# Performance work log

Measured on AMD Instinct MI355X. Metric: run time of the kernel, lower is better.

## Reference

```python
import jax, jax.numpy as jnp
import numpy as np
from jax import lax

EPS = 1e-5


def _conv3x3(inp, w):
    # NCHW input, OIHW kernel, VALID padding, stride 1 (matches nn.Conv2d(k=3, s=1, p=0))
    return lax.conv_general_dilated(inp, w, (1, 1), 'VALID',
                                    dimension_numbers=('NCHW', 'OIHW', 'NCHW'))


def _bn(h, gamma, beta, mean, var):
    # inference-mode BatchNorm2d
    inv = gamma / jnp.sqrt(var + EPS)
    return h * inv[None, :, None, None] + (beta - mean * inv)[None, :, None, None]


def _xcorr_depthwise(zf, xf):
    # per-sample, per-channel sliding cross-correlation: template zf over search xf
    B, C, Hz, Wz = zf.shape
    _, _, Hx, Wx = xf.shape
    xr = xf.reshape(1, B * C, Hx, Wx)
    kr = zf.reshape(B * C, 1, Hz, Wz)
    out = lax.conv_general_dilated(xr, kr, (1, 1), 'VALID',
                                   feature_group_count=B * C,
                                   dimension_numbers=('NCHW', 'OIHW', 'NCHW'))
    return out.reshape(B, C, out.shape[2], out.shape[3])


def setup_inputs() -> dict:
    key = jax.random.key(0)
    ks = jax.random.split(key, 12)
    B, Cin, Ch = 64, 256, 256
    z = jax.random.normal(ks[0], (B, Cin, 16, 16), dtype=jnp.float32)
    x = jax.random.normal(ks[1], (B, Cin, 32, 32), dtype=jnp.float32)
    # conv weights ~ N(0, 0.01) as in _initialize_weights
    w_z = 0.01 * jax.random.normal(ks[2], (Ch, Cin, 3, 3), dtype=jnp.float32)
    w_x = 0.01 * jax.random.normal(ks[3], (Ch, Cin, 3, 3), dtype=jnp.float32)
    gamma_z = 0.5 + jax.random.uniform(ks[4], (Ch,), dtype=jnp.float32)
    beta_z = 0.1 * jax.random.normal(ks[5], (Ch,), dtype=jnp.float32)
    mean_z = 0.1 * jax.random.normal(ks[6], (Ch,), dtype=jnp.float32)
    var_z = 0.5 + jax.random.uniform(ks[7], (Ch,), dtype=jnp.float32)
    gamma_x = 0.5 + jax.random.uniform(ks[8], (Ch,), dtype=jnp.float32)
    beta_x = 0.1 * jax.random.normal(ks[9], (Ch,), dtype=jnp.float32)
    mean_x = 0.1 * jax.random.normal(ks[10], (Ch,), dtype=jnp.float32)
    var_x = 0.5 + jax.random.uniform(ks[11], (Ch,), dtype=jnp.float32)
    return {'z': z, 'x': x, 'w_z': w_z, 'w_x': w_x,
            'gamma_z': gamma_z, 'beta_z': beta_z, 'mean_z': mean_z, 'var_z': var_z,
            'gamma_x': gamma_x, 'beta_x': beta_x, 'mean_x': mean_x, 'var_x': var_x}


def reference(z, x, w_z, w_x, gamma_z, beta_z, mean_z, var_z,
              gamma_x, beta_x, mean_x, var_x):
    zf = _bn(_conv3x3(z, w_z), gamma_z, beta_z, mean_z, var_z)   # [B,C,14,14]
    xf = _bn(_conv3x3(x, w_x), gamma_x, beta_x, mean_x, var_x)   # [B,C,30,30]
    return _xcorr_depthwise(zf, xf)                               # [B,C,17,17]
```

## Files before the change

### kernel.cpp

```cpp
#include <hip/hip_runtime.h>
#include <cstdint>
#include <cstddef>

typedef _Float16 f16;
typedef _Float16 half4 __attribute__((ext_vector_type(4)));
typedef _Float16 half8 __attribute__((ext_vector_type(8)));
typedef __fp16 fp16x2 __attribute__((ext_vector_type(2)));
typedef float f32x4 __attribute__((ext_vector_type(4)));

#define BN_EPS 1e-5f

#if defined(__has_builtin)
# if __has_builtin(__builtin_amdgcn_fdot2)
#  define HAVE_FDOT2 1
# endif
#endif
#ifndef HAVE_FDOT2
# define HAVE_FDOT2 0
#endif

static constexpr size_t OFF_XB  = 0;
static constexpr size_t OFF_ZB  = 33554432;
static constexpr size_t OFF_WX  = 41943040;
static constexpr size_t OFF_WZ  = 43122688;
static constexpr size_t OFF_BNX = 44302336;
static constexpr size_t OFF_BNZ = 44304384;
static constexpr size_t OFF_XFH = 44306432;
static constexpr size_t OFF_ZFH = 75763712;

__global__ __launch_bounds__(256) void prep_all(
    const float* __restrict__ x, const float* __restrict__ z,
    const float* __restrict__ w_x, const float* __restrict__ w_z,
    const float* __restrict__ gx, const float* __restrict__ bx,
    const float* __restrict__ mx, const float* __restrict__ vx,
    const float* __restrict__ gz, const float* __restrict__ bz,
    const float* __restrict__ mz, const float* __restrict__ vz,
    f16* __restrict__ xb, f16* __restrict__ zb,
    f16* __restrict__ wxA, f16* __restrict__ wzA,
    float* __restrict__ bnx, float* __restrict__ bnz) {
  __shared__ float tile[64][33];
  __shared__ alignas(16) f16 wtile[2304];
  const int bid = blockIdx.x;
  const int tid = threadIdx.x;
  if (bid < 12288) {
    const float* src; f16* dst; int lw, r;
    if (bid < 8192) { src = x; dst = xb; lw = 5; r = bid; }
    else            { src = z; dst = zb; lw = 4; r = bid - 8192; }
    const int W = 1 << lw;
    const int c0 = (r & 3) << 6;
    const int h = (r >> 2) & (W - 1);
    const int b = (r >> 2) >> lw;
    const float* sp = src + ((size_t)((b << 8) + c0) << (2 * lw)) + ((size_t)h << lw);
    const int w4 = W >> 2;
    const int n1 = w4 << 6;
    for (int i = tid; i < n1; i += 256) {
      int cl = i >> (lw - 2), c4 = i & (w4 - 1);
      float4 v = *(const float4*)(sp + ((size_t)cl << (2 * lw)) + (c4 << 2));
      int w0 = c4 << 2;
      tile[cl][w0] = v.x; tile[cl][w0 + 1] = v.y;
      tile[cl][w0 + 2] = v.z; tile[cl][w0 + 3] = v.w;
    }
    __syncthreads();
    f16* dp = dst + ((size_t)((b << lw) + h) << lw << 8) + c0;
    const int n2 = W << 3;
    for (int j = tid; j < n2; j += 256) {
      int w = j >> 3, cl0 = (j & 7) << 3;
      half8 o;
#pragma unroll
      for (int e = 0; e < 8; ++e) o[e] = (f16)tile[cl0 + e][w];
      *(half8*)(dp + (w << 8) + cl0) = o;
    }
  } else if (bid < 12800) {
    int r = bid - 12288;
    const float* src = (r < 256) ? w_x : w_z;
    f16* dst = (r < 256) ? wxA : wzA;
    int cout = r & 255;
    const float* sp = src + (size_t)cout * 2304;
    for (int i = tid; i < 2304; i += 256) {
      int cin = i / 9, khw = i - cin * 9;
      wtile[khw * 256 + cin] = (f16)sp[i];
    }
    __syncthreads();
    for (int c = tid; c < 288; c += 256) {
      int khw = c >> 5, cin0 = (c & 31) << 3;
      *(half8*)(dst + (khw << 16) + (cout << 8) + cin0) =
          *(const half8*)(wtile + khw * 256 + cin0);
    }
  } else {
    int c = tid;
    float iv = gx[c] / sqrtf(vx[c] + BN_EPS);
    bnx[c] = iv;
    bnx[256 + c] = bx[c] - mx[c] * iv;
    float iz = gz[c] / sqrtf(vz[c] + BN_EPS);
    bnz[c] = iz;
    bnz[256 + c] = bz[c] - mz[c] * iz;
  }
}

__device__ __forceinline__ void gl_lds16(const f16* g, f16* l) {
  __builtin_amdgcn_global_load_lds((__attribute__((address_space(1))) void*)g,
                                   (__attribute__((address_space(3))) void*)l, 16, 0, 0);
}

__global__ __launch_bounds__(256, 4) void conv_gemm_u(
    const f16* __restrict__ xb, const f16* __restrict__ zb,
    const f16* __restrict__ wx, const f16* __restrict__ wz,
    const float* __restrict__ bnx, const float* __restrict__ bnz,
    f16* __restrict__ xfh, f16* __restrict__ zfh) {
  __shared__ f16 As[128 * 64];
  __shared__ f16 Bs[128 * 64];
  const int g = blockIdx.x;
  const int pairIdx = ((g >> 4) << 3) | (g & 7);
  const int mblk = (g >> 3) & 1;
  if (pairIdx >= 548) return;
  const f16* inp; const f16* wA; const float* bn; f16* out;
  int nblk, HIN, WIN, WOUT, NPIX, WPAD, OPLANE;
  if (pairIdx < 450) {
    inp = xb; wA = wx; bn = bnx; out = xfh; nblk = pairIdx;
    HIN = 32; WIN = 32; WOUT = 30; NPIX = 900; WPAD = 32; OPLANE = 960;
  } else {
    inp = zb; wA = wz; bn = bnz; out = zfh; nblk = pairIdx - 450;
    HIN = 16; WIN = 16; WOUT = 14; NPIX = 196; WPAD = 16; OPLANE = 224;
  }
  const int tid = threadIdx.x;
  const int wid = tid >> 6, lane = tid & 63;
  const int wm = (wid >> 1) << 6, wn = (wid & 1) << 6;
  const int q = lane >> 4, lm = lane & 15;
  const int sr = lane >> 3, sc = lane & 7;
  const int swz = (sc ^ sr) << 3;
  const int mbase = mblk << 7;

  int arow[4], brow[4];
#pragma unroll
  for (int l = 0; l < 4; ++l) {
    int rr = (wid << 5) + (l << 3) + sr;
    arow[l] = ((mbase + rr) << 8) + swz;
    int n = (nblk << 7) + rr;
    int b = n / NPIX, rem = n - b * NPIX;
    int oh = rem / WOUT, ow = rem - oh * WOUT;
    brow[l] = (((b * HIN + oh) * WIN + ow) << 8) + swz;
  }

  f32x4 acc[4][4] = {};
  const int cA0 = (q ^ (lm & 7)) << 3;

  for (int kt = 0; kt < 36; ++kt) {
    const int cinb = kt / 9;
    const int khw = kt - cinb * 9;
    const int cin0 = cinb << 6;
    const int kh = khw / 3, kw = khw - kh * 3;
    const int wofs = (khw << 16) + cin0;
    const int iofs = ((kh * WIN + kw) << 8) + cin0;
#pragma unroll
    for (int l = 0; l < 4; ++l) {
      const int ldso = ((wid << 5) + (l << 3)) << 6;
      gl_lds16(wA + wofs + arow[l], As + ldso);
      gl_lds16(inp + iofs + brow[l], Bs + ldso);
    }
    __syncthreads();
#pragma unroll
    for (int h = 0; h < 2; ++h) {
      const int co = cA0 ^ (h << 5);
      half8 af[4], bf[4];
#pragma unroll
      for (int f = 0; f < 4; ++f) {
        af[f] = *(const half8*)&As[((wm + (f << 4) + lm) << 6) + co];
        bf[f] = *(const half8*)&Bs[((wn + (f << 4) + lm) << 6) + co];
      }
#pragma unroll
      for (int fm = 0; fm < 4; ++fm)
#pragma unroll
        for (int fn = 0; fn < 4; ++fn)
          acc[fm][fn] =
              __builtin_amdgcn_mfma_f32_16x16x32_f16(af[fm], bf[fn], acc[fm][fn], 0, 0, 0);
    }
    __syncthreads();
  }

#pragma unroll
  for (int fn = 0; fn < 4; ++fn) {
    int n_g = (nblk << 7) + wn + (fn << 4) + lm;
    int b = n_g / NPIX, rem = n_g - b * NPIX;
    int oh = rem / WOUT, ow = rem - oh * WOUT;
    f16* op = out + (size_t)(b << 8) * OPLANE + oh * WPAD + ow;
#pragma unroll
    for (int fm = 0; fm < 4; ++fm) {
      int m0 = mbase + wm + (fm << 4) + (q << 2);
#pragma unroll
      for (int rg = 0; rg < 4; ++rg) {
        int m = m0 + rg;
        op[(size_t)m * OPLANE] = (f16)(acc[fm][fn][rg] * bn[m] + bn[256 + m]);
      }
    }
  }
}

static constexpr int XROWS = 30;
static constexpr int XSTR  = 40;
static constexpr int XCHN  = XROWS * XSTR;
static constexpr int ZCHN  = 224;
static constexpr int CPB   = 15;

__global__ __launch_bounds__(256) void xcorr_dw3(const f16* __restrict__ zfh,
                                                 const f16* __restrict__ xfh,
                                                 float* __restrict__ out) {
  __shared__ alignas(16) f16 xs[CPB * XCHN];
  __shared__ alignas(16) f16 zs[CPB * ZCHN];
  const int t = threadIdx.x;
  const int ch0 = blockIdx.x * CPB;

  for (int i = t; i < CPB * 30 * 4; i += 256) {
    int ch = i / 120, rem = i - ch * 120;
    int row = rem >> 2, c8 = (rem & 3) << 3;
    if (ch0 + ch < 16384)
      *(half8*)(xs + ch * XCHN + row * XSTR + c8) =
          *(const half8*)(xfh + (size_t)(ch0 + ch) * 960 + row * 32 + c8);
  }
  for (int i = t; i < CPB * 28; i += 256) {
    int ch = i / 28, rem = i - ch * 28;
    if (ch0 + ch < 16384)
      *(half8*)(zs + ch * ZCHN + rem * 8) =
          *(const half8*)(zfh + (size_t)(ch0 + ch) * 224 + rem * 8);
  }
  __syncthreads();

  int lc = t / 17;
  const int oy = t - lc * 17;
  const bool ok = (lc < CPB) && (ch0 + lc < 16384);
  if (lc >= CPB) lc = CPB - 1;
  const f16* xbp = xs + lc * XCHN;
  const f16* zbp = zs + lc * ZCHN;

  float acc[17];
#pragma unroll
  for (int j = 0; j < 17; ++j) acc[j] = 0.f;

#if HAVE_FDOT2
  union X32 { half8 v8[4]; fp16x2 h2[16]; };
  union Z16 { half8 v8[2]; fp16x2 h2[8]; };
  for (int u = 0; u < 14; ++u) {
    X32 xl;
#pragma unroll
    for (int k = 0; k < 4; ++k)
      xl.v8[k] = *(const half8*)(xbp + (oy + u) * XSTR + (k << 3));
    Z16 zl;
    zl.v8[0] = *(const half8*)(zbp + u * 16);
    zl.v8[1] = *(const half8*)(zbp + u * 16 + 8);
    fp16x2 xo[15];
#pragma unroll
    for (int m = 0; m < 15; ++m) { xo[m][0] = xl.h2[m][1]; xo[m][1] = xl.h2[m + 1][0]; }
#pragma unroll
    for (int m = 0; m < 7; ++m) {
#pragma unroll
      for (int tt = 0; tt < 8; ++tt) {
        acc[2 * tt]     = __builtin_amdgcn_fdot2(zl.h2[m], xl.h2[m + tt], acc[2 * tt], false);
        acc[2 * tt + 1] = __builtin_amdgcn_fdot2(zl.h2[m], xo[m + tt],    acc[2 * tt + 1], false);
      }
      acc[16] = __builtin_amdgcn_fdot2(zl.h2[m], xl.h2[m + 8], acc[16], false);
    }
  }
#else
  for (int u = 0; u < 14; ++u) {
    float xr[30];
#pragma unroll
    for (int k = 0; k < 4; ++k) {
      half8 h = *(const half8*)(xbp + (oy + u) * XSTR + (k << 3));
#pragma unroll
      for (int e = 0; e < 8; ++e)
        if (k * 8 + e < 30) xr[k * 8 + e] = (float)h[e];
    }
    float zc[14];
    {
      half8 z0 = *(const half8*)(zbp + u * 16);
      half8 z1 = *(const half8*)(zbp + u * 16 + 8);
#pragma unroll
      for (int e = 0; e < 8; ++e) zc[e] = (float)z0[e];
#pragma unroll
      for (int e = 0; e < 6; ++e) zc[8 + e] = (float)z1[e];
    }
#pragma unroll
    for (int v = 0; v < 14; ++v)
#pragma unroll
      for (int j = 0; j < 17; ++j) acc[j] = fmaf(zc[v], xr[v + j], acc[j]);
  }
#endif

  if (ok) {
    float* op = out + (size_t)(ch0 + lc) * 289 + oy * 17;
#pragma unroll
    for (int j = 0; j < 17; ++j) op[j] = acc[j];
  }
}

extern "C" void kernel_launch(void* const* d_in, const int* in_sizes, int n_in,
                              void* d_out, int out_size, void* d_ws, size_t ws_size,
                              hipStream_t stream) {
  const float* z = (const float*)d_in[0];
  const float* x = (const float*)d_in[1];
  const float* w_z = (const float*)d_in[2];
  const float* w_x = (const float*)d_in[3];
  const float* gamma_z = (const float*)d_in[4];
  const float* beta_z = (const float*)d_in[5];
  const float* mean_z = (const float*)d_in[6];
  const float* var_z = (const float*)d_in[7];
  const float* gamma_x = (const float*)d_in[8];
  const float* beta_x = (const float*)d_in[9];
  const float* mean_x = (const float*)d_in[10];
  const float* var_x = (const float*)d_in[11];

  char* ws = (char*)d_ws;
  f16* xb = (f16*)(ws + OFF_XB);
  f16* zb = (f16*)(ws + OFF_ZB);
  f16* wxA = (f16*)(ws + OFF_WX);
  f16* wzA = (f16*)(ws + OFF_WZ);
  float* bnx = (float*)(ws + OFF_BNX);
  float* bnz = (float*)(ws + OFF_BNZ);
  f16* xfh = (f16*)(ws + OFF_XFH);
  f16* zfh = (f16*)(ws + OFF_ZFH);
  float* out = (float*)d_out;

  prep_all<<<12801, 256, 0, stream>>>(x, z, w_x, w_z,
                                      gamma_x, beta_x, mean_x, var_x,
                                      gamma_z, beta_z, mean_z, var_z,
                                      xb, zb, wxA, wzA, bnx, bnz);

  conv_gemm_u<<<1104, 256, 0, stream>>>(xb, zb, wxA, wzA, bnx, bnz, xfh, zfh);

  xcorr_dw3<<<(16384 + CPB - 1) / CPB, 256, 0, stream>>>(zfh, xfh, out);
}
```

Baseline: 276.0 us.

## Stage input row band once per cin block and reuse across 3x3 taps

The implicit-GEMM conv now loads a contiguous band of input pixel rows (256 rows x 64 channels) into LDS once per 64-channel block. All 9 kernel taps are served from that band by shifting row offsets, so the input is no longer reloaded per tap. Weights are read straight from global memory into registers instead of going through LDS. Tiles are now per batch and row segment, which gives 1280 blocks with tail masking, and launch bounds are lowered to 3 waves per SIMD. This trades more LDS per block and more global weight traffic for far fewer input loads and barriers.

```diff
diff --git a/kernel.cpp b/kernel.cpp
--- a/kernel.cpp
+++ b/kernel.cpp
@@ -102,94 +102,112 @@
                                    (__attribute__((address_space(3))) void*)l, 16, 0, 0);
 }
 
-__global__ __launch_bounds__(256, 4) void conv_gemm_u(
+__global__ __launch_bounds__(256, 3) void conv_gemm_u(
     const f16* __restrict__ xb, const f16* __restrict__ zb,
     const f16* __restrict__ wx, const f16* __restrict__ wz,
     const float* __restrict__ bnx, const float* __restrict__ bnz,
     f16* __restrict__ xfh, f16* __restrict__ zfh) {
-  __shared__ f16 As[128 * 64];
-  __shared__ f16 Bs[128 * 64];
+  __shared__ alignas(16) f16 Bs[256 * 64];
   const int g = blockIdx.x;
   const int pairIdx = ((g >> 4) << 3) | (g & 7);
   const int mblk = (g >> 3) & 1;
-  if (pairIdx >= 548) return;
   const f16* inp; const f16* wA; const float* bn; f16* out;
-  int nblk, HIN, WIN, WOUT, NPIX, WPAD, OPLANE;
-  if (pairIdx < 450) {
-    inp = xb; wA = wx; bn = bnx; out = xfh; nblk = pairIdx;
+  int b, t, HIN, WIN, WOUT, NPIX, WPAD, OPLANE;
+  if (pairIdx < 512) {
+    inp = xb; wA = wx; bn = bnx; out = xfh;
+    b = pairIdx >> 3; t = pairIdx & 7;
     HIN = 32; WIN = 32; WOUT = 30; NPIX = 900; WPAD = 32; OPLANE = 960;
   } else {
-    inp = zb; wA = wz; bn = bnz; out = zfh; nblk = pairIdx - 450;
+    int r = pairIdx - 512;
+    inp = zb; wA = wz; bn = bnz; out = zfh;
+    b = r >> 1; t = r & 1;
     HIN = 16; WIN = 16; WOUT = 14; NPIX = 196; WPAD = 16; OPLANE = 224;
   }
   const int tid = threadIdx.x;
   const int wid = tid >> 6, lane = tid & 63;
   const int wm = (wid >> 1) << 6, wn = (wid & 1) << 6;
   const int q = lane >> 4, lm = lane & 15;
-  const int sr = lane >> 3, sc = lane & 7;
-  const int swz = (sc ^ sr) << 3;
   const int mbase = mblk << 7;
 
-  int arow[4], brow[4];
-#pragma unroll
-  for (int l = 0; l < 4; ++l) {
-    int rr = (wid << 5) + (l << 3) + sr;
-    arow[l] = ((mbase + rr) << 8) + swz;
-    int n = (nblk << 7) + rr;
-    int b = n / NPIX, rem = n - b * NPIX;
-    int oh = rem / WOUT, ow = rem - oh * WOUT;
-    brow[l] = (((b * HIN + oh) * WIN + ow) << 8) + swz;
-  }
+  const int ih0 = (t << 7) / WOUT;
+  const int pix0 = b * HIN * WIN + ih0 * WIN;
+
+  int inrow[4];
+#pragma unroll
+  for (int fn = 0; fn < 4; ++fn) {
+    int n_out = (t << 7) + wn + (fn << 4) + lm;
+    int v = n_out < NPIX ? n_out : NPIX - 1;
+    int oh = v / WOUT, ow = v - oh * WOUT;
+    inrow[fn] = (oh - ih0) * WIN + ow;
+  }
+
+  const f16* Abase = wA + ((mbase + wm + lm) << 8) + (q << 3);
 
   f32x4 acc[4][4] = {};
-  const int cA0 = (q ^ (lm & 7)) << 3;
-
-  for (int kt = 0; kt < 36; ++kt) {
-    const int cinb = kt / 9;
-    const int khw = kt - cinb * 9;
-    const int cin0 = cinb << 6;
-    const int kh = khw / 3, kw = khw - kh * 3;
-    const int wofs = (khw << 16) + cin0;
-    const int iofs = ((kh * WIN + kw) << 8) + cin0;
-#pragma unroll
-    for (int l = 0; l < 4; ++l) {
-      const int ldso = ((wid << 5) + (l << 3)) << 6;
-      gl_lds16(wA + wofs + arow[l], As + ldso);
-      gl_lds16(inp + iofs + brow[l], Bs + ldso);
-    }
+  const int cb0 = q << 4;
+  const int cb1 = (4 + q) << 4;
+
+  for (int cinb = 0; cinb < 4; ++cinb) {
     __syncthreads();
 #pragma unroll
-    for (int h = 0; h < 2; ++h) {
-      const int co = cA0 ^ (h << 5);
-      half8 af[4], bf[4];
-#pragma unroll
-      for (int f = 0; f < 4; ++f) {
-        af[f] = *(const half8*)&As[((wm + (f << 4) + lm) << 6) + co];
-        bf[f] = *(const half8*)&Bs[((wn + (f << 4) + lm) << 6) + co];
+    for (int i = 0; i < 8; ++i) {
+      int c = i * 256 + tid;
+      int r = c >> 3, s = c & 7;
+      int gc = s ^ (r & 7);
+      gl_lds16(inp + ((size_t)(pix0 + r) << 8) + (cinb << 6) + (gc << 3),
+               Bs + (size_t)c * 8);
+    }
+    __syncthreads();
+
+    const f16* Ak = Abase + (cinb << 6);
+#pragma unroll
+    for (int khw = 0; khw < 9; ++khw) {
+      const int kh = khw / 3, kw = khw - kh * 3;
+      const int koff = kh * WIN + kw;
+      half8 af[4][2];
+#pragma unroll
+      for (int f = 0; f < 4; ++f)
+#pragma unroll
+        for (int h = 0; h < 2; ++h)
+          af[f][h] = *(const half8*)(Ak + (khw << 16) + (f << 12) + (h << 5));
+      int rb[4], rx[4];
+#pragma unroll
+      for (int fn = 0; fn < 4; ++fn) {
+        int r = inrow[fn] + koff;
+        rb[fn] = r << 7;
+        rx[fn] = (r & 7) << 4;
       }
 #pragma unroll
-      for (int fm = 0; fm < 4; ++fm)
+      for (int h = 0; h < 2; ++h) {
+        const int cb = h ? cb1 : cb0;
+        half8 bf[4];
 #pragma unroll
         for (int fn = 0; fn < 4; ++fn)
-          acc[fm][fn] =
-              __builtin_amdgcn_mfma_f32_16x16x32_f16(af[fm], bf[fn], acc[fm][fn], 0, 0, 0);
-    }
-    __syncthreads();
+          bf[fn] = *(const half8*)((const char*)Bs + rb[fn] + (cb ^ rx[fn]));
+#pragma unroll
+        for (int fm = 0; fm < 4; ++fm)
+#pragma unroll
+          for (int fn = 0; fn < 4; ++fn)
+            acc[fm][fn] = __builtin_amdgcn_mfma_f32_16x16x32_f16(
+                af[fm][h], bf[fn], acc[fm][fn], 0, 0, 0);
+      }
+    }
   }
 
 #pragma unroll
   for (int fn = 0; fn < 4; ++fn) {
-    int n_g = (nblk << 7) + wn + (fn << 4) + lm;
-    int b = n_g / NPIX, rem = n_g - b * NPIX;
-    int oh = rem / WOUT, ow = rem - oh * WOUT;
-    f16* op = out + (size_t)(b << 8) * OPLANE + oh * WPAD + ow;
-#pragma unroll
-    for (int fm = 0; fm < 4; ++fm) {
-      int m0 = mbase + wm + (fm << 4) + (q << 2);
-#pragma unroll
-      for (int rg = 0; rg < 4; ++rg) {
-        int m = m0 + rg;
-        op[(size_t)m * OPLANE] = (f16)(acc[fm][fn][rg] * bn[m] + bn[256 + m]);
+    int n_out = (t << 7) + wn + (fn << 4) + lm;
+    if (n_out < NPIX) {
+      int oh = n_out / WOUT, ow = n_out - oh * WOUT;
+      f16* op = out + (size_t)(b << 8) * OPLANE + oh * WPAD + ow;
+#pragma unroll
+      for (int fm = 0; fm < 4; ++fm) {
+        int m0 = mbase + wm + (fm << 4) + (q << 2);
+#pragma unroll
+        for (int rg = 0; rg < 4; ++rg) {
+          int m = m0 + rg;
+          op[(size_t)m * OPLANE] = (f16)(acc[fm][fn][rg] * bn[m] + bn[256 + m]);
+        }
       }
     }
   }
@@ -324,7 +342,7 @@
                                       gamma_z, beta_z, mean_z, var_z,
                                       xb, zb, wxA, wzA, bnx, bnz);
 
-  conv_gemm_u<<<1104, 256, 0, stream>>>(xb, zb, wxA, wzA, bnx, bnz, xfh, zfh);
+  conv_gemm_u<<<1280, 256, 0, stream>>>(xb, zb, wxA, wzA, bnx, bnz, xfh, zfh);
 
   xcorr_dw3<<<(16384 + CPB - 1) / CPB, 256, 0, stream>>>(zfh, xfh, out);
 }
```

After: 436.5 us. 1.58x slower.
